# Optimization experiments

Hardware: AMD Instinct MI355X
Metric: run time of the kernel (lower is better)

The kernel has to match this reference:

```python
import jax, jax.numpy as jnp
import numpy as np

V_TEXT = 256
V_TOTAL = 4352
B, H, TQ, TK = 8, 4, 800, 128
T_TOK = 1024
BLANK_LOGPROB = -8.0
NEG = -1e9  # finite stand-in for -inf (keeps grads nan-free)
CE_W = 1.5
ATTN_W = 10.0
ATTN_START = 5000


def setup_inputs() -> dict:
    key = jax.random.key(0)
    ks = jax.random.split(key, 6)
    logits = jax.random.normal(ks[0], (B, T_TOK, V_TOTAL), dtype=jnp.float32)
    attn_logprob = jax.random.normal(ks[1], (B, H, TQ, TK), dtype=jnp.float32)
    token_targets = jax.random.randint(ks[2], (B, T_TOK), V_TEXT, V_TOTAL, dtype=jnp.int32)
    audio_target_lens = jax.random.randint(ks[3], (B,), 512, T_TOK + 1, dtype=jnp.int32)
    src_lens = jax.random.randint(ks[4], (B,), 64, TK + 1, dtype=jnp.int32)  # key (text) lens
    out_lens = jax.random.randint(ks[5], (B,), 400, TQ + 1, dtype=jnp.int32)  # query (audio) lens
    return {"logits": logits, "attn_logprob": attn_logprob, "token_targets": token_targets,
            "audio_target_lens": audio_target_lens, "src_lens": src_lens, "out_lens": out_lens,
            "current_step": 6000}


def _masked_ce(logits, targets, valid_mask):
    # CE over the audio slice of the shared vocab; pads ignored; divide by mask count.
    v_audio = logits.shape[-1] - V_TEXT
    logp = jax.nn.log_softmax(logits[:, :, V_TEXT:], axis=-1)  # (B,T,Va)
    tgt = targets - V_TEXT
    valid = valid_mask & (targets != -100)
    safe = jnp.clip(tgt, 0, v_audio - 1)
    nll = -jnp.take_along_axis(logp, safe[..., None], axis=-1)[..., 0]  # (B,T)
    loss_sum = jnp.sum(jnp.where(valid, nll, 0.0))
    denom = jnp.maximum(jnp.sum(valid_mask), 1).astype(logp.dtype)
    return loss_sum / denom


def _forward_sum(attn_logprob, key_lens, query_lens):
    # Batched CTC forward-sum over all (batch, head) pairs.
    # Targets for item b are 1..K_b (all distinct), blank = class 0 (padded logit -8).
    Bb, Hh, Tq, Tk = attn_logprob.shape
    N = Bb * Hh
    lp = jnp.pad(attn_logprob, ((0, 0), (0, 0), (0, 0), (1, 0)), constant_values=BLANK_LOGPROB)
    lp = lp.reshape(N, Tq, Tk + 1)
    klens = jnp.repeat(key_lens, Hh)    # (N,)
    qlens = jnp.repeat(query_lens, Hh)  # (N,)
    # masked log_softmax over the first K_b+1 classes only (matches per-item slice)
    cls_valid = jnp.arange(Tk + 1)[None, None, :] < (klens[:, None, None] + 1)
    logp = jax.nn.log_softmax(jnp.where(cls_valid, lp, NEG), axis=-1)  # (N,Tq,Tk+1)

    S = 2 * Tk + 1
    s = jnp.arange(S)
    ext_label = jnp.where(s % 2 == 1, (s + 1) // 2, 0)       # blank,1,blank,2,...
    skip_ok = (s % 2 == 1) & (s >= 2)                        # labels distinct -> skip always ok
    ext_valid = s[None, :] < (2 * klens[:, None] + 1)        # (N,S)
    emit = logp[:, :, ext_label]                             # (N,Tq,S)

    alpha0 = jnp.full((N, S), NEG, dtype=logp.dtype)
    alpha0 = alpha0.at[:, 0].set(emit[:, 0, 0]).at[:, 1].set(emit[:, 0, 1])
    alpha0 = jnp.where(ext_valid, alpha0, NEG)

    def step(alpha, emit_t):
        sh1 = jnp.pad(alpha, ((0, 0), (1, 0)), constant_values=NEG)[:, :-1]
        sh2 = jnp.pad(alpha, ((0, 0), (2, 0)), constant_values=NEG)[:, :-2]
        sh2 = jnp.where(skip_ok[None, :], sh2, NEG)
        a = jnp.logaddexp(jnp.logaddexp(alpha, sh1), sh2) + emit_t
        a = jnp.where(ext_valid, a, NEG)
        return a, a

    _, alphas = jax.lax.scan(step, alpha0, jnp.moveaxis(emit[:, 1:], 1, 0))  # (Tq-1,N,S)
    alphas = jnp.concatenate([alpha0[None], alphas], axis=0)                 # (Tq,N,S)

    alpha_T = alphas[qlens - 1, jnp.arange(N)]  # (N,S) alpha at t = query_len-1
    e1 = jnp.take_along_axis(alpha_T, (2 * klens - 1)[:, None], axis=1)[:, 0]
    e2 = jnp.take_along_axis(alpha_T, (2 * klens)[:, None], axis=1)[:, 0]
    nll = -jnp.logaddexp(e1, e2)
    loss = nll / klens.astype(logp.dtype)  # torch CTCLoss 'mean' divides by target len
    loss = jnp.where(jnp.isfinite(loss) & (loss < 1e8), loss, 0.0)  # zero_infinity
    return jnp.mean(loss)  # == sum_b/B then sum_h/H of the original loops


def _losses(logits, attn_logprob, token_targets, audio_target_lens, src_lens, out_lens, current_step):
    t_tok = token_targets.shape[1]
    valid = jnp.arange(t_tok)[None, :] < audio_target_lens[:, None]
    token_loss = _masked_ce(logits, token_targets, valid)
    if current_step > ATTN_START:
        q = jnp.minimum(out_lens, attn_logprob.shape[2])
        k = jnp.minimum(src_lens, attn_logprob.shape[3])
        attn_loss = _forward_sum(attn_logprob, k, q)
    else:
        attn_loss = jnp.zeros((), dtype=logits.dtype)
    total = token_loss * CE_W + attn_loss * ATTN_W
    return jnp.stack([total, attn_loss, token_loss])


def reference(logits, attn_logprob, token_targets, audio_target_lens, src_lens, out_lens, current_step):
    return _losses(logits, attn_logprob, token_targets, audio_target_lens, src_lens, out_lens, current_step)
```

## Files before the change

### kernel.cpp

```cpp
#include <hip/hip_runtime.h>
#include <cstdint>
#include <cstddef>

#define V_TEXT   256
#define V_TOTAL  4352
#define V_AUDIO  4096
#define B_       8
#define TQ_      800
#define TK_      128
#define T_TOK    1024
#define NSEQ     32
#define K2       1.4426950408889634f
#define LN2      0.6931471805599453f
#define EM8      3.3546262790251185e-04f
#define FNEGINF  (-3.0e38f)
#define CHK      32
#define NBUF     3

template <int CTRL>
__device__ __forceinline__ float dpp_mov(float x, float old) {
    return __int_as_float(__builtin_amdgcn_update_dpp(
        __float_as_int(old), __float_as_int(x), CTRL, 0xf, 0xf, false));
}
__device__ __forceinline__ float dpp_shr1_old(float x, float old) {
    return dpp_mov<0x138>(x, old);
}
__device__ __forceinline__ float lane_bcast(float x, int lane) {
    return __int_as_float(__builtin_amdgcn_readlane(__float_as_int(x), lane));
}
__device__ __forceinline__ float wave_max(float x) {
    x = fmaxf(x, dpp_mov<0x111>(x, FNEGINF));
    x = fmaxf(x, dpp_mov<0x112>(x, FNEGINF));
    x = fmaxf(x, dpp_mov<0x114>(x, FNEGINF));
    x = fmaxf(x, dpp_mov<0x118>(x, FNEGINF));
    x = fmaxf(x, dpp_mov<0x142>(x, FNEGINF));
    x = fmaxf(x, dpp_mov<0x143>(x, FNEGINF));
    return lane_bcast(x, 63);
}

__device__ __forceinline__ void lds_barrier() {
    asm volatile("s_waitcnt lgkmcnt(0)" ::: "memory");
    __builtin_amdgcn_s_barrier();
    asm volatile("" ::: "memory");
}

__device__ __forceinline__ void load6(float4* v, const float* __restrict__ abase,
                                      int g0, int pw, int lane) {
    int half = lane >> 5, col = (lane & 31) * 4;
    int i0 = pw * 5;
    #pragma unroll
    for (int u = 0; u < 6; u++) {
        int rc = min(g0 + 2 * (i0 + u) + half, TQ_ - 1);
        v[u] = *reinterpret_cast<const float4*>(abase + (size_t)rc * TK_ + col);
    }
}

__device__ __forceinline__ void write6(float* db, const float4* v, int g0, int pw,
                                       int k, int q, int lane, float& prod, int& acc) {
    int half = lane >> 5, col = (lane & 31) * 4;
    int i0 = pw * 5;
    #pragma unroll
    for (int u = 0; u < 6; u++) {
        int r  = 2 * (i0 + u) + half;
        int rg = g0 + r;
        float e0 = (col + 0 < k) ? __builtin_exp2f(v[u].x * K2) : 0.0f;
        float e1 = (col + 1 < k) ? __builtin_exp2f(v[u].y * K2) : 0.0f;
        float e2 = (col + 2 < k) ? __builtin_exp2f(v[u].z * K2) : 0.0f;
        float e3 = (col + 3 < k) ? __builtin_exp2f(v[u].w * K2) : 0.0f;
        *reinterpret_cast<float4*>(db + r * TK_ + col) = make_float4(e0, e1, e2, e3);

        float ps = (e0 + e1) + (e2 + e3);
        ps += dpp_mov<0x111>(ps, 0.0f);
        ps += dpp_mov<0x112>(ps, 0.0f);
        ps += dpp_mov<0x114>(ps, 0.0f);
        ps += dpp_mov<0x118>(ps, 0.0f);
        ps += dpp_mov<0x142>(ps, 0.0f);
        ps += EM8;
        bool owned = (u < 5) || (pw == 2);
        prod *= (owned && rg < q) ? ps : 1.0f;
        if (u & 1) {
            int b = __float_as_int(prod);
            acc += (b >> 23) - 127;
            prod = __int_as_float((b & 0x007fffff) | 0x3f800000);
        }
    }
}

__global__ __launch_bounds__(256) void fused_kernel(
    const float* __restrict__ logits, const int* __restrict__ targets,
    const int* __restrict__ alens,
    const float* __restrict__ attn, const int* __restrict__ slens,
    const int* __restrict__ olens,
    float* __restrict__ nll_out, float* __restrict__ loss_out)
{
    __shared__ float buf[NBUF][CHK][TK_];
    __shared__ float cshp[4];

    int tid = threadIdx.x;
    int wid = tid >> 6, lane = tid & 63;

    if (blockIdx.x >= NSEQ) {
        int row = (blockIdx.x - NSEQ) * 4 + wid;
        const float* p = logits + (size_t)row * V_TOTAL + V_TEXT;

        float4 v0 = *reinterpret_cast<const float4*>(p + lane * 4);
        float4 v1 = *reinterpret_cast<const float4*>(p + lane * 4 + 1024);
        float4 v2 = *reinterpret_cast<const float4*>(p + lane * 4 + 2048);
        float4 v3 = *reinterpret_cast<const float4*>(p + lane * 4 + 3072);
        int tg = targets[row];

        float m = fmaxf(fmaxf(fmaxf(v0.x, v0.y), fmaxf(v0.z, v0.w)),
                        fmaxf(fmaxf(v1.x, v1.y), fmaxf(v1.z, v1.w)));
        m = fmaxf(m, fmaxf(fmaxf(v2.x, v2.y), fmaxf(v2.z, v2.w)));
        m = fmaxf(m, fmaxf(fmaxf(v3.x, v3.y), fmaxf(v3.z, v3.w)));
        m = wave_max(m);

        float mn = -m * K2;
        float s =
          __builtin_exp2f(__builtin_fmaf(v0.x,K2,mn)) + __builtin_exp2f(__builtin_fmaf(v0.y,K2,mn))
        + __builtin_exp2f(__builtin_fmaf(v0.z,K2,mn)) + __builtin_exp2f(__builtin_fmaf(v0.w,K2,mn))
        + __builtin_exp2f(__builtin_fmaf(v1.x,K2,mn)) + __builtin_exp2f(__builtin_fmaf(v1.y,K2,mn))
        + __builtin_exp2f(__builtin_fmaf(v1.z,K2,mn)) + __builtin_exp2f(__builtin_fmaf(v1.w,K2,mn))
        + __builtin_exp2f(__builtin_fmaf(v2.x,K2,mn)) + __builtin_exp2f(__builtin_fmaf(v2.y,K2,mn))
        + __builtin_exp2f(__builtin_fmaf(v2.z,K2,mn)) + __builtin_exp2f(__builtin_fmaf(v2.w,K2,mn))
        + __builtin_exp2f(__builtin_fmaf(v3.x,K2,mn)) + __builtin_exp2f(__builtin_fmaf(v3.y,K2,mn))
        + __builtin_exp2f(__builtin_fmaf(v3.z,K2,mn)) + __builtin_exp2f(__builtin_fmaf(v3.w,K2,mn));
        s += dpp_mov<0x111>(s, 0.0f);
        s += dpp_mov<0x112>(s, 0.0f);
        s += dpp_mov<0x114>(s, 0.0f);
        s += dpp_mov<0x118>(s, 0.0f);
        s += dpp_mov<0x142>(s, 0.0f);
        s  = lane_bcast(s, 31) + lane_bcast(s, 63);

        if (lane == 0) {
            float lse = m + __builtin_log2f(s) * LN2;
            int b = row >> 10, t = row & (T_TOK - 1);
            bool valid = (t < alens[b]) && (tg != -100);
            float nll = 0.0f;
            if (valid) {
                int idx = min(max(tg - V_TEXT, 0), V_AUDIO - 1);
                nll = lse - p[idx];
            }
            nll_out[row] = nll;
        }
        return;
    }

    int n = blockIdx.x;
    int k = min(slens[n >> 2], TK_);
    int q = min(olens[n >> 2], TQ_);
    int ncha = (q + CHK - 1) / CHK;
    const float* abase = attn + (size_t)n * TQ_ * TK_;

    float prod = 1.0f;
    int   acc  = 0;

    float p0 = (wid == 0 && lane == 0) ? 1.0f : 0.0f;
    float p1 = 0.0f, p2 = 0.0f, p3 = 0.0f, p4 = 0.0f, p3s = 0.0f;
    int   Mtot = 0;

    float4 R0[6], R1[6];

    if (wid > 0) {
        load6(R0, abase, 0,       wid - 1, lane);
        load6(R1, abase, CHK,     wid - 1, lane);
        write6(&buf[0][0][0], R0, 0, wid - 1, k, q, lane, prod, acc);
        load6(R0, abase, 2 * CHK, wid - 1, lane);
    }
    lds_barrier();

#define SSTEP(xv)                                                            \
    do {                                                                     \
        float c01 = p0 + p3s;                                                \
        float c12 = p2 + p1;                                                 \
        float n4  = (p4 + p3) * EM8;                                         \
        p0 = c01 * EM8;                                                      \
        p1 = (p1 + c01) * xv.x;                                              \
        p2 = c12 * EM8;                                                      \
        p3 = (p3 + c12) * xv.y;                                              \
        p4 = n4;                                                             \
        p3s = dpp_shr1_old(p3, 0.0f);                                        \
    } while (0)

    for (int c = 0; c < ncha; c++) {
        if (wid > 0) {
            if (c + 1 < ncha) {
                float* db = &buf[(c + 1) % NBUF][0][0];
                if ((c + 1) & 1) write6(db, R1, (c + 1) * CHK, wid - 1, k, q, lane, prod, acc);
                else             write6(db, R0, (c + 1) * CHK, wid - 1, k, q, lane, prod, acc);
            }
            if (c + 3 < ncha) {
                if ((c + 3) & 1) load6(R1, abase, (c + 3) * CHK, wid - 1, lane);
                else             load6(R0, abase, (c + 3) * CHK, wid - 1, lane);
            }
        } else {
            const float* lb = &buf[c % NBUF][0][2 * lane];
            int lim = min(CHK, q - c * CHK);
            int nfull = lim >> 3, rem = lim & 7;
            float2 cur[8], nxt[8];
            #pragma unroll
            for (int j = 0; j < 8; j++)
                cur[j] = *reinterpret_cast<const float2*>(lb + min(j, CHK - 1) * TK_);
            for (int g = 0; g < nfull; g++) {
                int base = g * 8;
                #pragma unroll
                for (int j = 0; j < 8; j++)
                    nxt[j] = *reinterpret_cast<const float2*>(lb + min(base + 8 + j, CHK - 1) * TK_);
                float wm = fmaxf(fmaxf(fmaxf(p0, p1), fmaxf(p2, p3)),
                                 fmaxf(p4, p3s));
                #pragma unroll
                for (int j = 0; j < 8; j++) SSTEP(cur[j]);
                wm = fmaxf(wm, dpp_mov<0x111>(wm, FNEGINF));
                wm = fmaxf(wm, dpp_mov<0x112>(wm, FNEGINF));
                wm = fmaxf(wm, dpp_mov<0x114>(wm, FNEGINF));
                wm = fmaxf(wm, dpp_mov<0x118>(wm, FNEGINF));
                wm = fmaxf(wm, dpp_mov<0x142>(wm, FNEGINF));
                wm = fmaxf(wm, dpp_mov<0x143>(wm, FNEGINF));
                wm = lane_bcast(wm, 63);
                int ebits = __float_as_int(wm) & 0x7f800000;
                if (ebits > 0) {
                    int se = 222 - (ebits >> 23);
                    se = se < 1 ? 1 : (se > 254 ? 254 : se);
                    float sc = __int_as_float(se << 23);
                    Mtot += 127 - se;
                    p0 *= sc; p1 *= sc; p2 *= sc; p3 *= sc; p4 *= sc; p3s *= sc;
                }
                #pragma unroll
                for (int j = 0; j < 8; j++) cur[j] = nxt[j];
            }
            #pragma unroll
            for (int j = 0; j < 8; j++) if (j < rem) SSTEP(cur[j]);
        }
        lds_barrier();
    }
#undef SSTEP

    if (wid > 0) {
        float cl = __builtin_log2f(prod) + (float)acc;
        float cs = lane_bcast(cl, 31) + lane_bcast(cl, 63);
        if (lane == 0) cshp[wid] = cs;
    }
    __syncthreads();

    if (wid == 0) {
        float csh = cshp[1] + cshp[2] + cshp[3];
        int s1 = 2 * k - 1, s2 = 2 * k;
        float e1v, e2v;
        {
            int l = s1 >> 2, r = s1 & 3;
            float c1 = __shfl(p1, l), c3 = __shfl(p3, l);
            e1v = (r == 1) ? c1 : c3;
        }
        if (s2 == 256) {
            e2v = __shfl(p4, 63);
        } else {
            int l = s2 >> 2, r = s2 & 3;
            float c0 = __shfl(p0, l), c2 = __shfl(p2, l);
            e2v = (r == 0) ? c0 : c2;
        }
        float l2 = __builtin_log2f(e1v + e2v) + (float)Mtot - csh;
        float nll = -l2 * LN2;
        float loss = nll / (float)k;
        if (!(isfinite(loss) && loss < 1.0e8f)) loss = 0.0f;
        if (lane == 0) loss_out[n] = loss;
    }
}

__global__ __launch_bounds__(256) void fin_kernel(
    const float* __restrict__ nll, const int* __restrict__ alens,
    const int* __restrict__ step, const float* __restrict__ attn_losses,
    float* __restrict__ out)
{
    __shared__ float red[4];
    int tid = threadIdx.x;
    float s = 0.0f;
    for (int i = tid; i < B_ * T_TOK; i += 256) s += nll[i];
    #pragma unroll
    for (int off = 32; off > 0; off >>= 1) s += __shfl_xor(s, off);
    if ((tid & 63) == 0) red[tid >> 6] = s;
    __syncthreads();
    if (tid == 0) {
        float ce_sum = red[0] + red[1] + red[2] + red[3];
        int denom = 0;
        for (int b = 0; b < B_; b++) denom += min(alens[b], T_TOK);
        denom = max(denom, 1);
        float token = ce_sum / (float)denom;
        float a = 0.0f;
        for (int i = 0; i < NSEQ; i++) a += attn_losses[i];
        a *= (1.0f / NSEQ);
        if (step[0] <= 5000) a = 0.0f;
        out[0] = 1.5f * token + 10.0f * a;
        out[1] = a;
        out[2] = token;
    }
}

extern "C" void kernel_launch(void* const* d_in, const int* in_sizes, int n_in,
                              void* d_out, int out_size, void* d_ws, size_t ws_size,
                              hipStream_t stream)
{
    const float* logits  = (const float*)d_in[0];
    const float* attn    = (const float*)d_in[1];
    const int*   targets = (const int*)d_in[2];
    const int*   alens   = (const int*)d_in[3];
    const int*   slens   = (const int*)d_in[4];
    const int*   olens   = (const int*)d_in[5];
    const int*   step    = (const int*)d_in[6];
    float* out = (float*)d_out;
    float* ws  = (float*)d_ws;

    float* ws_attn = ws;
    float* ws_nll  = ws + 64;

    fused_kernel<<<dim3(NSEQ + B_ * T_TOK / 4), dim3(256), 0, stream>>>(
        logits, targets, alens, attn, slens, olens, ws_nll, ws_attn);
    fin_kernel<<<dim3(1), dim3(256), 0, stream>>>(ws_nll, alens, step, ws_attn, out);
}
```

Measured before the change: 236.9 us.

## Split emission exponentiation into a parallel pre-pass and stream it via global_load_lds

Emission exponentiation for the attention CTC moves out of the 32 serial recurrence blocks and into 200 extra blocks of the CE kernel, which write exp(attn) to a workspace buffer. A separate recurrence kernel then copies chunks straight into LDS with global_load_lds, using 64-row chunks and double buffering, while the producer waves compute the row-sum normalisers from LDS. The goal is to shorten the latency-bound recurrence critical path by taking the exp work off it. In exchange it adds a full workspace write and read of about 13 MB and one extra kernel launch. The old fused path is kept as a fallback when the workspace is too small.

```diff
diff --git a/kernel.cpp b/kernel.cpp
--- a/kernel.cpp
+++ b/kernel.cpp
@@ -14,8 +14,11 @@
 #define LN2      0.6931471805599453f
 #define EM8      3.3546262790251185e-04f
 #define FNEGINF  (-3.0e38f)
-#define CHK      32
-#define NBUF     3
+#define CHK      64
+#define NBUF     2
+#define NCE      2048
+#define NEMIS    200
+#define EMIS_FLOATS (NSEQ * TQ_ * TK_)
 
 template <int CTRL>
 __device__ __forceinline__ float dpp_mov(float x, float old) {
@@ -37,70 +40,33 @@
     x = fmaxf(x, dpp_mov<0x143>(x, FNEGINF));
     return lane_bcast(x, 63);
 }
-
-__device__ __forceinline__ void lds_barrier() {
-    asm volatile("s_waitcnt lgkmcnt(0)" ::: "memory");
-    __builtin_amdgcn_s_barrier();
-    asm volatile("" ::: "memory");
-}
-
-__device__ __forceinline__ void load6(float4* v, const float* __restrict__ abase,
-                                      int g0, int pw, int lane) {
-    int half = lane >> 5, col = (lane & 31) * 4;
-    int i0 = pw * 5;
-    #pragma unroll
-    for (int u = 0; u < 6; u++) {
-        int rc = min(g0 + 2 * (i0 + u) + half, TQ_ - 1);
-        v[u] = *reinterpret_cast<const float4*>(abase + (size_t)rc * TK_ + col);
-    }
-}
-
-__device__ __forceinline__ void write6(float* db, const float4* v, int g0, int pw,
-                                       int k, int q, int lane, float& prod, int& acc) {
-    int half = lane >> 5, col = (lane & 31) * 4;
-    int i0 = pw * 5;
-    #pragma unroll
-    for (int u = 0; u < 6; u++) {
-        int r  = 2 * (i0 + u) + half;
-        int rg = g0 + r;
-        float e0 = (col + 0 < k) ? __builtin_exp2f(v[u].x * K2) : 0.0f;
-        float e1 = (col + 1 < k) ? __builtin_exp2f(v[u].y * K2) : 0.0f;
-        float e2 = (col + 2 < k) ? __builtin_exp2f(v[u].z * K2) : 0.0f;
-        float e3 = (col + 3 < k) ? __builtin_exp2f(v[u].w * K2) : 0.0f;
-        *reinterpret_cast<float4*>(db + r * TK_ + col) = make_float4(e0, e1, e2, e3);
-
-        float ps = (e0 + e1) + (e2 + e3);
-        ps += dpp_mov<0x111>(ps, 0.0f);
-        ps += dpp_mov<0x112>(ps, 0.0f);
-        ps += dpp_mov<0x114>(ps, 0.0f);
-        ps += dpp_mov<0x118>(ps, 0.0f);
-        ps += dpp_mov<0x142>(ps, 0.0f);
-        ps += EM8;
-        bool owned = (u < 5) || (pw == 2);
-        prod *= (owned && rg < q) ? ps : 1.0f;
-        if (u & 1) {
-            int b = __float_as_int(prod);
-            acc += (b >> 23) - 127;
-            prod = __int_as_float((b & 0x007fffff) | 0x3f800000);
-        }
-    }
-}
-
-__global__ __launch_bounds__(256) void fused_kernel(
+__device__ __forceinline__ float wave_sum(float x) {
+    x += dpp_mov<0x111>(x, 0.0f);
+    x += dpp_mov<0x112>(x, 0.0f);
+    x += dpp_mov<0x114>(x, 0.0f);
+    x += dpp_mov<0x118>(x, 0.0f);
+    x += dpp_mov<0x142>(x, 0.0f);
+    x += dpp_mov<0x143>(x, 0.0f);
+    return lane_bcast(x, 63);
+}
+
+__device__ __forceinline__ void gll16(const float* g, float* l) {
+    __builtin_amdgcn_global_load_lds(
+        (const __attribute__((address_space(1))) void*)g,
+        (__attribute__((address_space(3))) void*)l, 16, 0, 0);
+}
+
+__global__ __launch_bounds__(256) void ce_emis_kernel(
     const float* __restrict__ logits, const int* __restrict__ targets,
     const int* __restrict__ alens,
     const float* __restrict__ attn, const int* __restrict__ slens,
-    const int* __restrict__ olens,
-    float* __restrict__ nll_out, float* __restrict__ loss_out)
+    float* __restrict__ nll_out, float* __restrict__ emis)
 {
-    __shared__ float buf[NBUF][CHK][TK_];
-    __shared__ float cshp[4];
-
     int tid = threadIdx.x;
     int wid = tid >> 6, lane = tid & 63;
 
-    if (blockIdx.x >= NSEQ) {
-        int row = (blockIdx.x - NSEQ) * 4 + wid;
+    if (blockIdx.x < NCE) {
+        int row = blockIdx.x * 4 + wid;
         const float* p = logits + (size_t)row * V_TOTAL + V_TEXT;
 
         float4 v0 = *reinterpret_cast<const float4*>(p + lane * 4);
@@ -125,12 +91,7 @@
         + __builtin_exp2f(__builtin_fmaf(v2.z,K2,mn)) + __builtin_exp2f(__builtin_fmaf(v2.w,K2,mn))
         + __builtin_exp2f(__builtin_fmaf(v3.x,K2,mn)) + __builtin_exp2f(__builtin_fmaf(v3.y,K2,mn))
         + __builtin_exp2f(__builtin_fmaf(v3.z,K2,mn)) + __builtin_exp2f(__builtin_fmaf(v3.w,K2,mn));
-        s += dpp_mov<0x111>(s, 0.0f);
-        s += dpp_mov<0x112>(s, 0.0f);
-        s += dpp_mov<0x114>(s, 0.0f);
-        s += dpp_mov<0x118>(s, 0.0f);
-        s += dpp_mov<0x142>(s, 0.0f);
-        s  = lane_bcast(s, 31) + lane_bcast(s, 63);
+        s = wave_sum(s);
 
         if (lane == 0) {
             float lse = m + __builtin_log2f(s) * LN2;
@@ -146,11 +107,38 @@
         return;
     }
 
-    int n = blockIdx.x;
+    unsigned b2 = blockIdx.x - NCE;
+    unsigned base = b2 * 16384u;
+    #pragma unroll
+    for (int u = 0; u < 16; u++) {
+        unsigned idx = base + (unsigned)(u * 256 + tid) * 4u;
+        float4 v = *reinterpret_cast<const float4*>(attn + idx);
+        int n   = (int)(idx / (unsigned)(TQ_ * TK_));
+        int col = (int)(idx & (TK_ - 1));
+        int k = min(slens[n >> 2], TK_);
+        float4 e;
+        e.x = (col     < k) ? __builtin_exp2f(v.x * K2) : 0.0f;
+        e.y = (col + 1 < k) ? __builtin_exp2f(v.y * K2) : 0.0f;
+        e.z = (col + 2 < k) ? __builtin_exp2f(v.z * K2) : 0.0f;
+        e.w = (col + 3 < k) ? __builtin_exp2f(v.w * K2) : 0.0f;
+        *reinterpret_cast<float4*>(emis + idx) = e;
+    }
+}
+
+__global__ __launch_bounds__(256) void rec_kernel(
+    const float* __restrict__ emis,
+    const int* __restrict__ slens, const int* __restrict__ olens,
+    float* __restrict__ loss_out)
+{
+    __shared__ float buf[NBUF][CHK][TK_];
+    __shared__ float cshp[4];
+    int n   = blockIdx.x;
+    int tid = threadIdx.x;
+    int wid = tid >> 6, lane = tid & 63;
     int k = min(slens[n >> 2], TK_);
     int q = min(olens[n >> 2], TQ_);
     int ncha = (q + CHK - 1) / CHK;
-    const float* abase = attn + (size_t)n * TQ_ * TK_;
+    const float* ebase = emis + (size_t)n * (TQ_ * TK_);
 
     float prod = 1.0f;
     int   acc  = 0;
@@ -159,15 +147,24 @@
     float p1 = 0.0f, p2 = 0.0f, p3 = 0.0f, p4 = 0.0f, p3s = 0.0f;
     int   Mtot = 0;
 
-    float4 R0[6], R1[6];
+#define STAGE(ch)                                                            \
+    do {                                                                     \
+        const float* gb = ebase + (size_t)(ch) * CHK * TK_;                  \
+        float* lb = &buf[(ch) & 1][0][0];                                    \
+        _Pragma("unroll")                                                    \
+        for (int u = 0; u < 11; u++) {                                       \
+            int kk = 3 * u + (wid - 1);                                      \
+            if (kk < 32 && (ch) * CHK + 2 * kk < TQ_)                        \
+                gll16(gb + kk * 256 + lane * 4, lb + kk * 256);              \
+        }                                                                    \
+    } while (0)
 
     if (wid > 0) {
-        load6(R0, abase, 0,       wid - 1, lane);
-        load6(R1, abase, CHK,     wid - 1, lane);
-        write6(&buf[0][0][0], R0, 0, wid - 1, k, q, lane, prod, acc);
-        load6(R0, abase, 2 * CHK, wid - 1, lane);
-    }
-    lds_barrier();
+        STAGE(0);
+        asm volatile("s_waitcnt vmcnt(0)" ::: "memory");
+    }
+    __builtin_amdgcn_s_barrier();
+    asm volatile("" ::: "memory");
 
 #define SSTEP(xv)                                                            \
     do {                                                                     \
@@ -184,28 +181,36 @@
 
     for (int c = 0; c < ncha; c++) {
         if (wid > 0) {
-            if (c + 1 < ncha) {
-                float* db = &buf[(c + 1) % NBUF][0][0];
-                if ((c + 1) & 1) write6(db, R1, (c + 1) * CHK, wid - 1, k, q, lane, prod, acc);
-                else             write6(db, R0, (c + 1) * CHK, wid - 1, k, q, lane, prod, acc);
-            }
-            if (c + 3 < ncha) {
-                if ((c + 3) & 1) load6(R1, abase, (c + 3) * CHK, wid - 1, lane);
-                else             load6(R0, abase, (c + 3) * CHK, wid - 1, lane);
-            }
+            if (c + 1 < ncha) STAGE(c + 1);
+            const float* cb = &buf[c & 1][0][0];
+            for (int i = 0; i < 22; i++) {
+                int r = (wid - 1) + 3 * i;
+                if (r >= CHK) break;
+                int rg = c * CHK + r;
+                float2 xv = *reinterpret_cast<const float2*>(cb + r * TK_ + 2 * lane);
+                float ps = wave_sum(xv.x + xv.y) + EM8;
+                prod *= (rg < q) ? ps : 1.0f;
+                if (i & 1) {
+                    int b = __float_as_int(prod);
+                    acc += (b >> 23) - 127;
+                    prod = __int_as_float((b & 0x007fffff) | 0x3f800000);
+                }
+            }
+            asm volatile("s_waitcnt vmcnt(0) lgkmcnt(0)" ::: "memory");
         } else {
-            const float* lb = &buf[c % NBUF][0][2 * lane];
+            const float* lb2 = &buf[c & 1][0][2 * lane];
             int lim = min(CHK, q - c * CHK);
             int nfull = lim >> 3, rem = lim & 7;
             float2 cur[8], nxt[8];
             #pragma unroll
             for (int j = 0; j < 8; j++)
-                cur[j] = *reinterpret_cast<const float2*>(lb + min(j, CHK - 1) * TK_);
+                cur[j] = *reinterpret_cast<const float2*>(lb2 + j * TK_);
             for (int g = 0; g < nfull; g++) {
                 int base = g * 8;
                 #pragma unroll
                 for (int j = 0; j < 8; j++)
-                    nxt[j] = *reinterpret_cast<const float2*>(lb + min(base + 8 + j, CHK - 1) * TK_);
+                    nxt[j] = *reinterpret_cast<const float2*>(
+                        lb2 + min(base + 8 + j, CHK - 1) * TK_);
                 float wm = fmaxf(fmaxf(fmaxf(p0, p1), fmaxf(p2, p3)),
                                  fmaxf(p4, p3s));
                 #pragma unroll
@@ -230,18 +235,224 @@
             }
             #pragma unroll
             for (int j = 0; j < 8; j++) if (j < rem) SSTEP(cur[j]);
+            asm volatile("s_waitcnt lgkmcnt(0)" ::: "memory");
+        }
+        __builtin_amdgcn_s_barrier();
+        asm volatile("" ::: "memory");
+    }
+#undef SSTEP
+#undef STAGE
+
+    if (wid > 0) {
+        float cl = __builtin_log2f(prod) + (float)acc;
+        if (lane == 0) cshp[wid] = cl;
+    }
+    __syncthreads();
+
+    if (wid == 0) {
+        float csh = cshp[1] + cshp[2] + cshp[3];
+        int s1 = 2 * k - 1, s2 = 2 * k;
+        float e1v, e2v;
+        {
+            int l = s1 >> 2, r = s1 & 3;
+            float c1 = __shfl(p1, l), c3 = __shfl(p3, l);
+            e1v = (r == 1) ? c1 : c3;
+        }
+        if (s2 == 256) {
+            e2v = __shfl(p4, 63);
+        } else {
+            int l = s2 >> 2, r = s2 & 3;
+            float c0 = __shfl(p0, l), c2 = __shfl(p2, l);
+            e2v = (r == 0) ? c0 : c2;
+        }
+        float l2 = __builtin_log2f(e1v + e2v) + (float)Mtot - csh;
+        float nll = -l2 * LN2;
+        float loss = nll / (float)k;
+        if (!(isfinite(loss) && loss < 1.0e8f)) loss = 0.0f;
+        if (lane == 0) loss_out[n] = loss;
+    }
+}
+
+__device__ __forceinline__ void lds_barrier() {
+    asm volatile("s_waitcnt lgkmcnt(0)" ::: "memory");
+    __builtin_amdgcn_s_barrier();
+    asm volatile("" ::: "memory");
+}
+__device__ __forceinline__ void load6(float4* v, const float* __restrict__ abase,
+                                      int g0, int pw, int lane) {
+    int half = lane >> 5, col = (lane & 31) * 4;
+    int i0 = pw * 5;
+    #pragma unroll
+    for (int u = 0; u < 6; u++) {
+        int rc = min(g0 + 2 * (i0 + u) + half, TQ_ - 1);
+        v[u] = *reinterpret_cast<const float4*>(abase + (size_t)rc * TK_ + col);
+    }
+}
+__device__ __forceinline__ void write6(float* db, const float4* v, int g0, int pw,
+                                       int k, int q, int lane, float& prod, int& acc) {
+    int half = lane >> 5, col = (lane & 31) * 4;
+    int i0 = pw * 5;
+    #pragma unroll
+    for (int u = 0; u < 6; u++) {
+        int r  = 2 * (i0 + u) + half;
+        int rg = g0 + r;
+        float e0 = (col + 0 < k) ? __builtin_exp2f(v[u].x * K2) : 0.0f;
+        float e1 = (col + 1 < k) ? __builtin_exp2f(v[u].y * K2) : 0.0f;
+        float e2 = (col + 2 < k) ? __builtin_exp2f(v[u].z * K2) : 0.0f;
+        float e3 = (col + 3 < k) ? __builtin_exp2f(v[u].w * K2) : 0.0f;
+        *reinterpret_cast<float4*>(db + r * TK_ + col) = make_float4(e0, e1, e2, e3);
+        float ps = (e0 + e1) + (e2 + e3);
+        ps += dpp_mov<0x111>(ps, 0.0f);
+        ps += dpp_mov<0x112>(ps, 0.0f);
+        ps += dpp_mov<0x114>(ps, 0.0f);
+        ps += dpp_mov<0x118>(ps, 0.0f);
+        ps += dpp_mov<0x142>(ps, 0.0f);
+        ps += EM8;
+        bool owned = (u < 5) || (pw == 2);
+        prod *= (owned && rg < q) ? ps : 1.0f;
+        if (u & 1) {
+            int b = __float_as_int(prod);
+            acc += (b >> 23) - 127;
+            prod = __int_as_float((b & 0x007fffff) | 0x3f800000);
+        }
+    }
+}
+#define FCHK 32
+__global__ __launch_bounds__(256) void fused_fallback(
+    const float* __restrict__ logits, const int* __restrict__ targets,
+    const int* __restrict__ alens,
+    const float* __restrict__ attn, const int* __restrict__ slens,
+    const int* __restrict__ olens,
+    float* __restrict__ nll_out, float* __restrict__ loss_out)
+{
+    __shared__ float buf[3][FCHK][TK_];
+    __shared__ float cshp[4];
+    int tid = threadIdx.x;
+    int wid = tid >> 6, lane = tid & 63;
+    if (blockIdx.x >= NSEQ) {
+        int row = (blockIdx.x - NSEQ) * 4 + wid;
+        const float* p = logits + (size_t)row * V_TOTAL + V_TEXT;
+        float4 v0 = *reinterpret_cast<const float4*>(p + lane * 4);
+        float4 v1 = *reinterpret_cast<const float4*>(p + lane * 4 + 1024);
+        float4 v2 = *reinterpret_cast<const float4*>(p + lane * 4 + 2048);
+        float4 v3 = *reinterpret_cast<const float4*>(p + lane * 4 + 3072);
+        int tg = targets[row];
+        float m = fmaxf(fmaxf(fmaxf(v0.x, v0.y), fmaxf(v0.z, v0.w)),
+                        fmaxf(fmaxf(v1.x, v1.y), fmaxf(v1.z, v1.w)));
+        m = fmaxf(m, fmaxf(fmaxf(v2.x, v2.y), fmaxf(v2.z, v2.w)));
+        m = fmaxf(m, fmaxf(fmaxf(v3.x, v3.y), fmaxf(v3.z, v3.w)));
+        m = wave_max(m);
+        float mn = -m * K2;
+        float s =
+          __builtin_exp2f(__builtin_fmaf(v0.x,K2,mn)) + __builtin_exp2f(__builtin_fmaf(v0.y,K2,mn))
+        + __builtin_exp2f(__builtin_fmaf(v0.z,K2,mn)) + __builtin_exp2f(__builtin_fmaf(v0.w,K2,mn))
+        + __builtin_exp2f(__builtin_fmaf(v1.x,K2,mn)) + __builtin_exp2f(__builtin_fmaf(v1.y,K2,mn))
+        + __builtin_exp2f(__builtin_fmaf(v1.z,K2,mn)) + __builtin_exp2f(__builtin_fmaf(v1.w,K2,mn))
+        + __builtin_exp2f(__builtin_fmaf(v2.x,K2,mn)) + __builtin_exp2f(__builtin_fmaf(v2.y,K2,mn))
+        + __builtin_exp2f(__builtin_fmaf(v2.z,K2,mn)) + __builtin_exp2f(__builtin_fmaf(v2.w,K2,mn))
+        + __builtin_exp2f(__builtin_fmaf(v3.x,K2,mn)) + __builtin_exp2f(__builtin_fmaf(v3.y,K2,mn))
+        + __builtin_exp2f(__builtin_fmaf(v3.z,K2,mn)) + __builtin_exp2f(__builtin_fmaf(v3.w,K2,mn));
+        s = wave_sum(s);
+        if (lane == 0) {
+            float lse = m + __builtin_log2f(s) * LN2;
+            int b = row >> 10, t = row & (T_TOK - 1);
+            bool valid = (t < alens[b]) && (tg != -100);
+            float nll = 0.0f;
+            if (valid) {
+                int idx = min(max(tg - V_TEXT, 0), V_AUDIO - 1);
+                nll = lse - p[idx];
+            }
+            nll_out[row] = nll;
+        }
+        return;
+    }
+    int n = blockIdx.x;
+    int k = min(slens[n >> 2], TK_);
+    int q = min(olens[n >> 2], TQ_);
+    int ncha = (q + FCHK - 1) / FCHK;
+    const float* abase = attn + (size_t)n * TQ_ * TK_;
+    float prod = 1.0f; int acc = 0;
+    float p0 = (wid == 0 && lane == 0) ? 1.0f : 0.0f;
+    float p1 = 0.0f, p2 = 0.0f, p3 = 0.0f, p4 = 0.0f, p3s = 0.0f;
+    int Mtot = 0;
+    float4 R0[6], R1[6];
+    if (wid > 0) {
+        load6(R0, abase, 0,        wid - 1, lane);
+        load6(R1, abase, FCHK,     wid - 1, lane);
+        write6(&buf[0][0][0], R0, 0, wid - 1, k, q, lane, prod, acc);
+        load6(R0, abase, 2 * FCHK, wid - 1, lane);
+    }
+    lds_barrier();
+#define SSTEP(xv)                                                            \
+    do {                                                                     \
+        float c01 = p0 + p3s;                                                \
+        float c12 = p2 + p1;                                                 \
+        float n4  = (p4 + p3) * EM8;                                         \
+        p0 = c01 * EM8;                                                      \
+        p1 = (p1 + c01) * xv.x;                                              \
+        p2 = c12 * EM8;                                                      \
+        p3 = (p3 + c12) * xv.y;                                              \
+        p4 = n4;                                                             \
+        p3s = dpp_shr1_old(p3, 0.0f);                                        \
+    } while (0)
+    for (int c = 0; c < ncha; c++) {
+        if (wid > 0) {
+            if (c + 1 < ncha) {
+                float* db = &buf[(c + 1) % 3][0][0];
+                if ((c + 1) & 1) write6(db, R1, (c + 1) * FCHK, wid - 1, k, q, lane, prod, acc);
+                else             write6(db, R0, (c + 1) * FCHK, wid - 1, k, q, lane, prod, acc);
+            }
+            if (c + 3 < ncha) {
+                if ((c + 3) & 1) load6(R1, abase, (c + 3) * FCHK, wid - 1, lane);
+                else             load6(R0, abase, (c + 3) * FCHK, wid - 1, lane);
+            }
+        } else {
+            const float* lb = &buf[c % 3][0][2 * lane];
+            int lim = min(FCHK, q - c * FCHK);
+            int nfull = lim >> 3, rem = lim & 7;
+            float2 cur[8], nxt[8];
+            #pragma unroll
+            for (int j = 0; j < 8; j++)
+                cur[j] = *reinterpret_cast<const float2*>(lb + min(j, FCHK - 1) * TK_);
+            for (int g = 0; g < nfull; g++) {
+                int base = g * 8;
+                #pragma unroll
+                for (int j = 0; j < 8; j++)
+                    nxt[j] = *reinterpret_cast<const float2*>(lb + min(base + 8 + j, FCHK - 1) * TK_);
+                float wm = fmaxf(fmaxf(fmaxf(p0, p1), fmaxf(p2, p3)),
+                                 fmaxf(p4, p3s));
+                #pragma unroll
+                for (int j = 0; j < 8; j++) SSTEP(cur[j]);
+                wm = fmaxf(wm, dpp_mov<0x111>(wm, FNEGINF));
+                wm = fmaxf(wm, dpp_mov<0x112>(wm, FNEGINF));
+                wm = fmaxf(wm, dpp_mov<0x114>(wm, FNEGINF));
+                wm = fmaxf(wm, dpp_mov<0x118>(wm, FNEGINF));
+                wm = fmaxf(wm, dpp_mov<0x142>(wm, FNEGINF));
+                wm = fmaxf(wm, dpp_mov<0x143>(wm, FNEGINF));
+                wm = lane_bcast(wm, 63);
+                int ebits = __float_as_int(wm) & 0x7f800000;
+                if (ebits > 0) {
+                    int se = 222 - (ebits >> 23);
+                    se = se < 1 ? 1 : (se > 254 ? 254 : se);
+                    float sc = __int_as_float(se << 23);
+                    Mtot += 127 - se;
+                    p0 *= sc; p1 *= sc; p2 *= sc; p3 *= sc; p4 *= sc; p3s *= sc;
+                }
+                #pragma unroll
+                for (int j = 0; j < 8; j++) cur[j] = nxt[j];
+            }
+            #pragma unroll
+            for (int j = 0; j < 8; j++) if (j < rem) SSTEP(cur[j]);
         }
         lds_barrier();
     }
 #undef SSTEP
-
     if (wid > 0) {
         float cl = __builtin_log2f(prod) + (float)acc;
         float cs = lane_bcast(cl, 31) + lane_bcast(cl, 63);
         if (lane == 0) cshp[wid] = cs;
     }
     __syncthreads();
-
     if (wid == 0) {
         float csh = cshp[1] + cshp[2] + cshp[3];
         int s1 = 2 * k - 1, s2 = 2 * k;
@@ -311,8 +522,17 @@
 
     float* ws_attn = ws;
     float* ws_nll  = ws + 64;
-
-    fused_kernel<<<dim3(NSEQ + B_ * T_TOK / 4), dim3(256), 0, stream>>>(
-        logits, targets, alens, attn, slens, olens, ws_nll, ws_attn);
+    float* ws_emis = ws + 16384;
+
+    size_t need = (size_t)(16384 + EMIS_FLOATS) * sizeof(float);
+    if (ws_size >= need) {
+        ce_emis_kernel<<<dim3(NCE + NEMIS), dim3(256), 0, stream>>>(
+            logits, targets, alens, attn, slens, ws_nll, ws_emis);
+        rec_kernel<<<dim3(NSEQ), dim3(256), 0, stream>>>(
+            ws_emis, slens, olens, ws_attn);
+    } else {
+        fused_fallback<<<dim3(NSEQ + NCE), dim3(256), 0, stream>>>(
+            logits, targets, alens, attn, slens, olens, ws_nll, ws_attn);
+    }
     fin_kernel<<<dim3(1), dim3(256), 0, stream>>>(ws_nll, alens, step, ws_attn, out);
 }
```

Result: slower. 260.9 us (+10.1%).
